# Kernel optimization log

Hardware: AMD Instinct MI355X
Metric: run time of the kernel (lower is better)

The kernel has to match this reference:

```python
import jax, jax.numpy as jnp
import numpy as np

B, L, C = 8, 3136, 192
HEADS, HEAD_CH = 3, 64
EPS = 1e-5


def _dwconv(x, w, s):
    # depthwise 3x3 conv, SAME padding; w: [3,3,1,C], feature_group_count=C
    return jax.lax.conv_general_dilated(
        x, w, (s, s), 'SAME',
        dimension_numbers=('NHWC', 'HWIO', 'NHWC'),
        feature_group_count=x.shape[-1])


def _proj(x, dw, scale, bias, mean, var, pw, s):
    # depthwise conv -> BN (inference, running stats) -> 1x1 pointwise conv
    h = _dwconv(x, dw, s)
    h = (h - mean) * jax.lax.rsqrt(var + EPS) * scale + bias
    return jax.lax.conv_general_dilated(
        h, pw, (1, 1), 'SAME',
        dimension_numbers=('NHWC', 'HWIO', 'NHWC'))


def setup_inputs() -> dict:
    key = jax.random.key(0)
    ks = jax.random.split(key, 7)
    d = {'x': jax.random.normal(ks[0], (B, L, C), jnp.float32)}
    for i, p in enumerate(['q', 'k', 'v']):
        d[p + '_dw'] = jax.random.normal(ks[i + 1], (3, 3, 1, C), jnp.float32) * 0.1
        d[p + '_scale'] = jnp.ones((C,), jnp.float32)
        d[p + '_bias'] = jnp.zeros((C,), jnp.float32)
        d[p + '_mean'] = jnp.zeros((C,), jnp.float32)
        d[p + '_var'] = jnp.ones((C,), jnp.float32)
        d[p + '_pw'] = jax.random.normal(ks[i + 4], (1, 1, C, HEADS * HEAD_CH), jnp.float32) * 0.05
    d['is_training'] = 0  # inference: BN uses running averages
    return d


def reference(x, q_dw, q_scale, q_bias, q_mean, q_var, q_pw,
              k_dw, k_scale, k_bias, k_mean, k_var, k_pw,
              v_dw, v_scale, v_bias, v_mean, v_var, v_pw,
              is_training):
    S = int(np.ceil(np.sqrt(L)))  # 56; L is a perfect square, so no token padding
    xi = x.reshape(B, S, S, C)
    q = _proj(xi, q_dw, q_scale, q_bias, q_mean, q_var, q_pw, 1)  # [B,56,56,192]
    k = _proj(xi, k_dw, k_scale, k_bias, k_mean, k_var, k_pw, 2)  # [B,28,28,192]
    v = _proj(xi, v_dw, v_scale, v_bias, v_mean, v_var, v_pw, 2)  # [B,28,28,192]
    q = q.reshape(B, -1, HEADS, HEAD_CH) / jnp.sqrt(jnp.float32(HEAD_CH))
    k = k.reshape(B, -1, HEADS, HEAD_CH)
    v = v.reshape(B, -1, HEADS, HEAD_CH)
    attn = jax.nn.softmax(jnp.einsum('bqhd,bkhd->bhqk', q, k), axis=-1)
    o = jnp.einsum('bhqk,bkhd->bqhd', attn, v)
    # num_heads*head_ch == out_ch -> plain head merge, no output projection
    return o.reshape(B, L, HEADS * HEAD_CH)
```

## Files before the change

kernel.cpp:

```cpp
#include <hip/hip_runtime.h>
#include <cmath>

#define EPS_BN 1e-5f

typedef __bf16 bf16;
typedef __bf16 bf16x4 __attribute__((ext_vector_type(4)));
typedef __bf16 bf16x8 __attribute__((ext_vector_type(8)));
typedef float  f32x4  __attribute__((ext_vector_type(4)));

__device__ __forceinline__ void dma16(const bf16* g, bf16* l) {
    __builtin_amdgcn_global_load_lds(
        (const __attribute__((address_space(1))) void*)g,
        (__attribute__((address_space(3))) void*)l, 16, 0, 0);
}

__global__ __launch_bounds__(256) void conv_all_kernel(
    const float* __restrict__ x,
    const float* __restrict__ qdw, const float* __restrict__ qscale,
    const float* __restrict__ qbias, const float* __restrict__ qmean,
    const float* __restrict__ qvar,
    const float* __restrict__ kdw, const float* __restrict__ kscale,
    const float* __restrict__ kbias, const float* __restrict__ kmean,
    const float* __restrict__ kvar,
    const float* __restrict__ vdw, const float* __restrict__ vscale,
    const float* __restrict__ vbias, const float* __restrict__ vmean,
    const float* __restrict__ vvar,
    const float* __restrict__ qpw, const float* __restrict__ kpw,
    const float* __restrict__ vpw,
    bf16* __restrict__ qhi, bf16* __restrict__ qlo,
    bf16* __restrict__ khi, bf16* __restrict__ klo,
    bf16* __restrict__ vhi, bf16* __restrict__ vlo,
    bf16* __restrict__ wt) {
    const int WW = 56, C = 192;
    int bid = blockIdx.x;

    if (bid < 4704) {
        int idx = bid * 256 + threadIdx.x;
        int p  = idx / 48;
        int c4 = (idx - p * 48) * 4;
        int b  = p / 3136;
        int rem = p - b * 3136;
        int oy = rem / 56;
        int ox = rem - oy * 56;
        const float* xb = x + (size_t)b * 3136 * C;

        float4 sc = *(const float4*)&qscale[c4];
        float4 vr = *(const float4*)&qvar[c4];
        float4 bi = *(const float4*)&qbias[c4];
        float4 mn = *(const float4*)&qmean[c4];
        float aA[4] = {sc.x * rsqrtf(vr.x + EPS_BN), sc.y * rsqrtf(vr.y + EPS_BN),
                       sc.z * rsqrtf(vr.z + EPS_BN), sc.w * rsqrtf(vr.w + EPS_BN)};
        float aB[4] = {bi.x - mn.x * aA[0], bi.y - mn.y * aA[1],
                       bi.z - mn.z * aA[2], bi.w - mn.w * aA[3]};
        float s[4] = {0.f, 0.f, 0.f, 0.f};
#pragma unroll
        for (int ky = 0; ky < 3; ky++) {
            int iy = oy + ky - 1;
            bool yok = (iy >= 0) && (iy < 56);
#pragma unroll
            for (int kx = 0; kx < 3; kx++) {
                int ix = ox + kx - 1;
                if (yok && ix >= 0 && ix < WW) {
                    float4 xv = *(const float4*)&xb[((size_t)iy * WW + ix) * C + c4];
                    float4 wv = *(const float4*)&qdw[(ky * 3 + kx) * C + c4];
                    s[0] += xv.x * wv.x; s[1] += xv.y * wv.y;
                    s[2] += xv.z * wv.z; s[3] += xv.w * wv.w;
                }
            }
        }
        bf16x4 hv, lv;
#pragma unroll
        for (int j = 0; j < 4; j++) {
            float av = s[j] * aA[j] + aB[j];
            bf16 hh = (bf16)av;
            hv[j] = hh;
            lv[j] = (bf16)(av - (float)hh);
        }
        *(bf16x4*)&qhi[(size_t)p * C + c4] = hv;
        *(bf16x4*)&qlo[(size_t)p * C + c4] = lv;
    } else if (bid < 5880) {
        int idx = (bid - 4704) * 256 + threadIdx.x;
        int p  = idx / 48;
        int c4 = (idx - p * 48) * 4;
        int b  = p / 784;
        int rem = p - b * 784;
        int oy = rem / 28;
        int ox = rem - oy * 28;
        const float* xb = x + (size_t)b * 3136 * C;

        float ks[4] = {0.f, 0.f, 0.f, 0.f};
        float vs[4] = {0.f, 0.f, 0.f, 0.f};
#pragma unroll
        for (int ky = 0; ky < 3; ky++) {
            int iy = oy * 2 + ky;
            bool yok = iy < 56;
#pragma unroll
            for (int kx = 0; kx < 3; kx++) {
                int ix = ox * 2 + kx;
                if (yok && ix < WW) {
                    float4 xv = *(const float4*)&xb[((size_t)iy * WW + ix) * C + c4];
                    float4 kw = *(const float4*)&kdw[(ky * 3 + kx) * C + c4];
                    float4 vw = *(const float4*)&vdw[(ky * 3 + kx) * C + c4];
                    ks[0] += xv.x * kw.x; ks[1] += xv.y * kw.y;
                    ks[2] += xv.z * kw.z; ks[3] += xv.w * kw.w;
                    vs[0] += xv.x * vw.x; vs[1] += xv.y * vw.y;
                    vs[2] += xv.z * vw.z; vs[3] += xv.w * vw.w;
                }
            }
        }
        float4 ksc = *(const float4*)&kscale[c4];
        float4 kvr = *(const float4*)&kvar[c4];
        float4 kbi = *(const float4*)&kbias[c4];
        float4 kmn = *(const float4*)&kmean[c4];
        float4 vsc = *(const float4*)&vscale[c4];
        float4 vvr = *(const float4*)&vvar[c4];
        float4 vbi = *(const float4*)&vbias[c4];
        float4 vmn = *(const float4*)&vmean[c4];
        float kA[4] = {ksc.x * rsqrtf(kvr.x + EPS_BN), ksc.y * rsqrtf(kvr.y + EPS_BN),
                       ksc.z * rsqrtf(kvr.z + EPS_BN), ksc.w * rsqrtf(kvr.w + EPS_BN)};
        float kB[4] = {kbi.x - kmn.x * kA[0], kbi.y - kmn.y * kA[1],
                       kbi.z - kmn.z * kA[2], kbi.w - kmn.w * kA[3]};
        float vA[4] = {vsc.x * rsqrtf(vvr.x + EPS_BN), vsc.y * rsqrtf(vvr.y + EPS_BN),
                       vsc.z * rsqrtf(vvr.z + EPS_BN), vsc.w * rsqrtf(vvr.w + EPS_BN)};
        float vB[4] = {vbi.x - vmn.x * vA[0], vbi.y - vmn.y * vA[1],
                       vbi.z - vmn.z * vA[2], vbi.w - vmn.w * vA[3]};
        bf16x4 kh, kl, vh, vl;
#pragma unroll
        for (int j = 0; j < 4; j++) {
            float kf = ks[j] * kA[j] + kB[j];
            float vf = vs[j] * vA[j] + vB[j];
            bf16 h1 = (bf16)kf; kh[j] = h1; kl[j] = (bf16)(kf - (float)h1);
            bf16 h2 = (bf16)vf; vh[j] = h2; vl[j] = (bf16)(vf - (float)h2);
        }
        *(bf16x4*)&khi[(size_t)p * C + c4] = kh;
        *(bf16x4*)&klo[(size_t)p * C + c4] = kl;
        *(bf16x4*)&vhi[(size_t)p * C + c4] = vh;
        *(bf16x4*)&vlo[(size_t)p * C + c4] = vl;
    } else {
        int idx = (bid - 5880) * 256 + threadIdx.x;
        if (idx < 3 * 36864) {
            int mat = idx / 36864, r = idx % 36864;
            int n = r / 192, k = r - n * 192;
            const float* src = (mat == 0) ? qpw : (mat == 1) ? kpw : vpw;
            wt[idx] = (bf16)src[k * 192 + n];
        }
    }
}

__global__ __launch_bounds__(256) void gemm_all_kernel(
    const bf16* __restrict__ qhi, const bf16* __restrict__ qlo,
    const bf16* __restrict__ khi, const bf16* __restrict__ klo,
    const bf16* __restrict__ vhi, const bf16* __restrict__ vlo,
    const bf16* __restrict__ wt,
    bf16* __restrict__ qbuf, bf16* __restrict__ kbuf, bf16* __restrict__ vtbuf) {
    __shared__ bf16 Ws[192][200];
    int t = threadIdx.x;
    int bid = blockIdx.x;

    int mode, mt;
    const bf16 *Ahi, *Alo, *Wsrc;
    if (bid < 392)      { mode = 0; mt = bid;       Ahi = qhi; Alo = qlo; Wsrc = wt; }
    else if (bid < 490) { mode = 1; mt = bid - 392; Ahi = khi; Alo = klo; Wsrc = wt + 36864; }
    else                { mode = 2; mt = bid - 490; Ahi = vhi; Alo = vlo; Wsrc = wt + 73728; }

#pragma unroll
    for (int it = 0; it < 18; it++) {
        int idx = it * 256 + t;
        int n = idx / 24, ck = idx - n * 24;
        *(uint4*)&Ws[n][ck * 8] = *(const uint4*)&Wsrc[n * 192 + ck * 8];
    }
    __syncthreads();

    int lane = t & 63, wid = t >> 6;
    int l16 = lane & 15, quad = lane >> 4;
    int wrow = wid * 16;
    int m0 = mt * 64;

    f32x4 acc[12];
#pragma unroll
    for (int n = 0; n < 12; n++) acc[n] = f32x4{0.f, 0.f, 0.f, 0.f};

    const bf16* arh = Ahi + (size_t)(m0 + wrow + l16) * 192;
    const bf16* arl = Alo + (size_t)(m0 + wrow + l16) * 192;
#pragma unroll
    for (int kc = 0; kc < 6; kc++) {
        bf16x8 ah = *(const bf16x8*)(arh + kc * 32 + quad * 8);
        bf16x8 al = *(const bf16x8*)(arl + kc * 32 + quad * 8);
#pragma unroll
        for (int n = 0; n < 12; n++) {
            bf16x8 bfr = *(const bf16x8*)&Ws[n * 16 + l16][kc * 32 + quad * 8];
            acc[n] = __builtin_amdgcn_mfma_f32_16x16x32_bf16(al, bfr, acc[n], 0, 0, 0);
            acc[n] = __builtin_amdgcn_mfma_f32_16x16x32_bf16(ah, bfr, acc[n], 0, 0, 0);
        }
    }

    if (mode == 2) {
#pragma unroll
        for (int reg = 0; reg < 4; reg++) {
            int row = m0 + wrow + quad * 4 + reg;
            int b = row / 784;
            int loc = row - b * 784;
#pragma unroll
            for (int n = 0; n < 12; n++) {
                int col = n * 16 + l16;
                int h = col >> 6, d = col & 63;
                vtbuf[(((size_t)b * 3 + h) * 64 + d) * 784 + loc] = (bf16)acc[n][reg];
            }
        }
    } else {
        bf16* outp = (mode == 0) ? qbuf : kbuf;
        const float s = (mode == 0) ? 0.125f : 1.0f;
#pragma unroll
        for (int reg = 0; reg < 4; reg++) {
            size_t row = m0 + wrow + quad * 4 + reg;
#pragma unroll
            for (int n = 0; n < 12; n++)
                outp[row * 192 + n * 16 + l16] = (bf16)(acc[n][reg] * s);
        }
    }
}

__global__ __launch_bounds__(256)
__attribute__((amdgpu_waves_per_eu(3, 3)))
void attn3_kernel(const bf16* __restrict__ qb,
                  const bf16* __restrict__ kb,
                  const bf16* __restrict__ vtb,
                  float* __restrict__ out) {
    const int LQ = 3136, LK = 784, C = 192;
    int qt = blockIdx.x, h = blockIdx.y, b = blockIdx.z;

    __shared__ bf16 Ks[8192];
    __shared__ bf16 Vts[64][136];
    __shared__ bf16 Ps[64][136];

    int t    = threadIdx.x;
    int lane = t & 63;
    int wid  = t >> 6;
    int l16  = lane & 15;
    int quad = lane >> 4;
    int wrow = wid * 16;

    if (t < 128) {
        int row = t >> 1, part = t & 1;
        *(uint4*)&Ps[row][112 + part * 8] = make_uint4(0u, 0u, 0u, 0u);
    }

    bf16x8 qfrag[2];
    {
        const bf16* qrow = qb + ((size_t)b * LQ + qt * 64 + wrow + l16) * C + h * 64;
        qfrag[0] = *(const bf16x8*)(qrow + quad * 8);
        qfrag[1] = *(const bf16x8*)(qrow + 32 + quad * 8);
    }

    const bf16* kbase  = kb + (size_t)b * LK * C + h * 64;
    const bf16* vtbase = vtb + ((size_t)(b * 3 + h)) * 64 * LK;

    float m_run = -INFINITY, l_run = 0.f;
    f32x4 o_acc[4];
#pragma unroll
    for (int dt = 0; dt < 4; dt++) o_acc[dt] = f32x4{0.f, 0.f, 0.f, 0.f};

    for (int c = 0; c < 7; c++) {
        int j0 = c * 112;
        __syncthreads();

        for (int s = wid; s < 33; s += 4) {
            if (s < 16) {
                int j = s * 64 + lane;
                int r = j / 9, cc = j - r * 9;
                const bf16* src = (cc < 8 && r < 112)
                                  ? kbase + (size_t)(j0 + r) * C + cc * 8
                                  : kbase;
                dma16(src, &Ks[s * 512]);
            } else {
                int s2 = s - 16;
                int j = s2 * 64 + lane;
                int r = j / 17, cc = j - r * 17;
                const bf16* src = (cc < 14)
                                  ? vtbase + (size_t)r * LK + j0 + cc * 8
                                  : vtbase;
                dma16(src, (bf16*)Vts + s2 * 512);
            }
        }
        __syncthreads();

        f32x4 st[7];
#pragma unroll
        for (int kb7 = 0; kb7 < 7; kb7++) st[kb7] = f32x4{0.f, 0.f, 0.f, 0.f};
#pragma unroll
        for (int kk = 0; kk < 2; kk++) {
#pragma unroll
            for (int kb7 = 0; kb7 < 7; kb7++) {
                bf16x8 afrag = *(const bf16x8*)&Ks[(kb7 * 16 + l16) * 72 + kk * 32 + quad * 8];
                st[kb7] = __builtin_amdgcn_mfma_f32_16x16x32_bf16(afrag, qfrag[kk], st[kb7], 0, 0, 0);
            }
        }

        float mx = -INFINITY;
#pragma unroll
        for (int kb7 = 0; kb7 < 7; kb7++)
#pragma unroll
            for (int r = 0; r < 4; r++) mx = fmaxf(mx, st[kb7][r]);
        mx = fmaxf(mx, __shfl_xor(mx, 16, 64));
        mx = fmaxf(mx, __shfl_xor(mx, 32, 64));
        float m_new = fmaxf(m_run, mx);
        float alpha = __expf(m_run - m_new);

        float rs = 0.f;
#pragma unroll
        for (int kb7 = 0; kb7 < 7; kb7++) {
            bf16x4 pv;
#pragma unroll
            for (int r = 0; r < 4; r++) {
                float p = __expf(st[kb7][r] - m_new);
                rs += p;
                pv[r] = (bf16)p;
            }
            *(bf16x4*)&Ps[wrow + l16][kb7 * 16 + quad * 4] = pv;
        }
        rs += __shfl_xor(rs, 16, 64);
        rs += __shfl_xor(rs, 32, 64);
        l_run = l_run * alpha + rs;
        m_run = m_new;
#pragma unroll
        for (int dt = 0; dt < 4; dt++)
#pragma unroll
            for (int r = 0; r < 4; r++) o_acc[dt][r] *= alpha;

#pragma unroll
        for (int kk = 0; kk < 4; kk++) {
            bf16x8 pfrag = *(const bf16x8*)&Ps[wrow + l16][kk * 32 + quad * 8];
#pragma unroll
            for (int dt = 0; dt < 4; dt++) {
                bf16x8 vfrag = *(const bf16x8*)&Vts[dt * 16 + l16][kk * 32 + quad * 8];
                o_acc[dt] = __builtin_amdgcn_mfma_f32_16x16x32_bf16(vfrag, pfrag, o_acc[dt], 0, 0, 0);
            }
        }
    }

    float invl = 1.f / l_run;
    float* ob = out + ((size_t)b * LQ + qt * 64 + wrow + l16) * C + h * 64;
#pragma unroll
    for (int dt = 0; dt < 4; dt++) {
        float4 v4 = {o_acc[dt][0] * invl, o_acc[dt][1] * invl,
                     o_acc[dt][2] * invl, o_acc[dt][3] * invl};
        *(float4*)(ob + dt * 16 + quad * 4) = v4;
    }
}

extern "C" void kernel_launch(void* const* d_in, const int* in_sizes, int n_in,
                              void* d_out, int out_size, void* d_ws, size_t ws_size,
                              hipStream_t stream) {
    const float* x = (const float*)d_in[0];

    const float* q_dw = (const float*)d_in[1];
    const float* q_scale = (const float*)d_in[2];
    const float* q_bias = (const float*)d_in[3];
    const float* q_mean = (const float*)d_in[4];
    const float* q_var = (const float*)d_in[5];
    const float* q_pw = (const float*)d_in[6];

    const float* k_dw = (const float*)d_in[7];
    const float* k_scale = (const float*)d_in[8];
    const float* k_bias = (const float*)d_in[9];
    const float* k_mean = (const float*)d_in[10];
    const float* k_var = (const float*)d_in[11];
    const float* k_pw = (const float*)d_in[12];

    const float* v_dw = (const float*)d_in[13];
    const float* v_scale = (const float*)d_in[14];
    const float* v_bias = (const float*)d_in[15];
    const float* v_mean = (const float*)d_in[16];
    const float* v_var = (const float*)d_in[17];
    const float* v_pw = (const float*)d_in[18];

    float* out = (float*)d_out;

    char* ws = (char*)d_ws;
    bf16* qhi = (bf16*)(ws);
    bf16* qlo = (bf16*)(ws + 9633792);
    bf16* khi = (bf16*)(ws + 19267584);
    bf16* klo = (bf16*)(ws + 21676032);
    bf16* vhi = (bf16*)(ws + 24084480);
    bf16* vlo = (bf16*)(ws + 26492928);
    bf16* qbuf = (bf16*)(ws + 28901376);
    bf16* kbuf = (bf16*)(ws + 38535168);
    bf16* vtbuf = (bf16*)(ws + 40943616);
    bf16* wt = (bf16*)(ws + 43352064);

    conv_all_kernel<<<6312, 256, 0, stream>>>(
        x,
        q_dw, q_scale, q_bias, q_mean, q_var,
        k_dw, k_scale, k_bias, k_mean, k_var,
        v_dw, v_scale, v_bias, v_mean, v_var,
        q_pw, k_pw, v_pw,
        qhi, qlo, khi, klo, vhi, vlo, wt);

    gemm_all_kernel<<<588, 256, 0, stream>>>(
        qhi, qlo, khi, klo, vhi, vlo, wt, qbuf, kbuf, vtbuf);

    attn3_kernel<<<dim3(49, 3, 8), 256, 0, stream>>>(qbuf, kbuf, vtbuf, out);
}
```

Before: 190.0 us.

## Load K/V MFMA fragments directly from global memory instead of LDS staging

```diff
diff --git a/kernel.cpp b/kernel.cpp
--- a/kernel.cpp
+++ b/kernel.cpp
@@ -7,12 +7,6 @@
 typedef __bf16 bf16x4 __attribute__((ext_vector_type(4)));
 typedef __bf16 bf16x8 __attribute__((ext_vector_type(8)));
 typedef float  f32x4  __attribute__((ext_vector_type(4)));
-
-__device__ __forceinline__ void dma16(const bf16* g, bf16* l) {
-    __builtin_amdgcn_global_load_lds(
-        (const __attribute__((address_space(1))) void*)g,
-        (__attribute__((address_space(3))) void*)l, 16, 0, 0);
-}
 
 __global__ __launch_bounds__(256) void conv_all_kernel(
     const float* __restrict__ x,
@@ -221,7 +215,7 @@
 }
 
 __global__ __launch_bounds__(256)
-__attribute__((amdgpu_waves_per_eu(3, 3)))
+__attribute__((amdgpu_waves_per_eu(4, 8)))
 void attn3_kernel(const bf16* __restrict__ qb,
                   const bf16* __restrict__ kb,
                   const bf16* __restrict__ vtb,
@@ -229,8 +223,6 @@
     const int LQ = 3136, LK = 784, C = 192;
     int qt = blockIdx.x, h = blockIdx.y, b = blockIdx.z;
 
-    __shared__ bf16 Ks[8192];
-    __shared__ bf16 Vts[64][136];
     __shared__ bf16 Ps[64][136];
 
     int t    = threadIdx.x;
@@ -240,8 +232,9 @@
     int quad = lane >> 4;
     int wrow = wid * 16;
 
-    if (t < 128) {
-        int row = t >> 1, part = t & 1;
+    if (lane < 32) {
+        int row = wrow + (lane >> 1);
+        int part = lane & 1;
         *(uint4*)&Ps[row][112 + part * 8] = make_uint4(0u, 0u, 0u, 0u);
     }
 
@@ -261,28 +254,9 @@
     for (int dt = 0; dt < 4; dt++) o_acc[dt] = f32x4{0.f, 0.f, 0.f, 0.f};
 
     for (int c = 0; c < 7; c++) {
-        int j0 = c * 112;
-        __syncthreads();
-
-        for (int s = wid; s < 33; s += 4) {
-            if (s < 16) {
-                int j = s * 64 + lane;
-                int r = j / 9, cc = j - r * 9;
-                const bf16* src = (cc < 8 && r < 112)
-                                  ? kbase + (size_t)(j0 + r) * C + cc * 8
-                                  : kbase;
-                dma16(src, &Ks[s * 512]);
-            } else {
-                int s2 = s - 16;
-                int j = s2 * 64 + lane;
-                int r = j / 17, cc = j - r * 17;
-                const bf16* src = (cc < 14)
-                                  ? vtbase + (size_t)r * LK + j0 + cc * 8
-                                  : vtbase;
-                dma16(src, (bf16*)Vts + s2 * 512);
-            }
-        }
-        __syncthreads();
+        const int j0 = c * 112;
+        const bf16* kc = kbase + (size_t)(j0 + l16) * C + quad * 8;
+        const bf16* vc = vtbase + (size_t)l16 * LK + j0 + quad * 8;
 
         f32x4 st[7];
 #pragma unroll
@@ -291,7 +265,7 @@
         for (int kk = 0; kk < 2; kk++) {
 #pragma unroll
             for (int kb7 = 0; kb7 < 7; kb7++) {
-                bf16x8 afrag = *(const bf16x8*)&Ks[(kb7 * 16 + l16) * 72 + kk * 32 + quad * 8];
+                bf16x8 afrag = *(const bf16x8*)(kc + (size_t)kb7 * 16 * C + kk * 32);
                 st[kb7] = __builtin_amdgcn_mfma_f32_16x16x32_bf16(afrag, qfrag[kk], st[kb7], 0, 0, 0);
             }
         }
@@ -332,7 +306,7 @@
             bf16x8 pfrag = *(const bf16x8*)&Ps[wrow + l16][kk * 32 + quad * 8];
 #pragma unroll
             for (int dt = 0; dt < 4; dt++) {
-                bf16x8 vfrag = *(const bf16x8*)&Vts[dt * 16 + l16][kk * 32 + quad * 8];
+                bf16x8 vfrag = *(const bf16x8*)(vc + (size_t)dt * 16 * LK + kk * 32);
                 o_acc[dt] = __builtin_amdgcn_mfma_f32_16x16x32_bf16(vfrag, pfrag, o_acc[dt], 0, 0, 0);
             }
         }
```

After: 224.4 us. +18.1%, slower.
